# Kernel optimization log

Measured on AMD Instinct MI355X. Metric: run time of the kernel, lower is better.

Reference implementation:

```python
import jax, jax.numpy as jnp
import numpy as np

B, NBLK, D, DY, NDIM, NMC, DH = 4096, 12, 2, 2, 24, 256, 100
SQRT3 = 3.0 ** 0.5
G2 = np.array([[1.0, 0.0], [0.5, SQRT3 / 2.0]], dtype=np.float32)
G = jnp.asarray(np.kron(np.eye(NBLK, dtype=np.float32), G2))  # (24,24) block-diag hexagonal generator
LOG_VOL = (NDIM // 2) * float(np.log(SQRT3 / 2.0))  # log sqrt(det(G G^T))


def _lin(x, w, b=None):
    y = x @ w.T
    return y if b is None else y + b


def _hex_quantize(y):
    # Exact nearest-point quantizer for the product-of-A2 (hexagonal) lattice.
    p = y.reshape(y.shape[:-1] + (NDIM // 2, 2))
    off = jnp.array([0.5, SQRT3 / 2.0], dtype=y.dtype)
    def rnd(q):  # round to rectangular sublattice Z x sqrt(3)Z
        return jnp.stack([jnp.round(q[..., 0]), jnp.round(q[..., 1] / SQRT3) * SQRT3], axis=-1)
    c0 = rnd(p)
    c1 = rnd(p - off) + off
    d0 = jnp.sum((p - c0) ** 2, axis=-1)
    d1 = jnp.sum((p - c1) ** 2, axis=-1)
    return jnp.where((d0 <= d1)[..., None], c0, c1).reshape(y.shape)


def _logits_cumulative(v, Hs, bs, fs):
    # compressai-style per-channel monotone cumulative network. v: (..., C) -> (..., C)
    v = v[..., None]  # (..., C, 1)
    for k in range(len(Hs)):
        v = jnp.einsum('coi,...ci->...co', jax.nn.softplus(Hs[k]), v) + bs[k][:, :, 0]
        if k < len(fs):
            v = v + jnp.tanh(fs[k][:, :, 0]) * jnp.tanh(v)
    return v[..., 0]


def setup_inputs() -> dict:
    key = jax.random.key(0)
    ks = iter(jax.random.split(key, 64))
    def nrm(shape, s=1.0):
        return jax.random.normal(next(ks), shape, jnp.float32) * s
    inp = {}
    inp['x'] = nrm((B, NBLK, D))
    inp['y_mean'] = nrm((NBLK, DY))
    inp['u'] = jax.random.uniform(next(ks), (NMC, NDIM), jnp.float32)
    inp['ga_w0'] = nrm((DH, D), D ** -0.5); inp['ga_b0'] = jnp.zeros((DH,), jnp.float32)
    inp['ga_w1'] = nrm((DH, DH), DH ** -0.5); inp['ga_b1'] = jnp.zeros((DH,), jnp.float32)
    inp['ga_w2'] = nrm((DY, DH), DH ** -0.5); inp['ga_b2'] = jnp.zeros((DY,), jnp.float32)
    inp['gs_w0'] = nrm((DH, DY), DY ** -0.5); inp['gs_b0'] = jnp.zeros((DH,), jnp.float32)
    inp['gs_w1'] = nrm((DH, DH), DH ** -0.5); inp['gs_b1'] = jnp.zeros((DH,), jnp.float32)
    inp['gs_w2'] = nrm((D, DH), DH ** -0.5); inp['gs_b2'] = jnp.zeros((D,), jnp.float32)
    inp['gac_w0'] = nrm((DH, NDIM), NDIM ** -0.5)
    inp['gac_w1'] = nrm((DH, DH), DH ** -0.5)
    inp['gac_w2'] = nrm((NDIM, DH), DH ** -0.5)
    inp['gsc_w0'] = nrm((DH, NDIM), NDIM ** -0.5)
    inp['gsc_w1'] = nrm((DH, DH), DH ** -0.5)
    inp['gsc_w2'] = nrm((NDIM, DH), DH ** -0.5)
    # factorized-prior cumulative params, layer dims 1->3->3->3->3->1
    inp['eb_H0'] = nrm((NDIM, 3, 1), 0.5)
    inp['eb_H1'] = nrm((NDIM, 3, 3), 0.5)
    inp['eb_H2'] = nrm((NDIM, 3, 3), 0.5)
    inp['eb_H3'] = nrm((NDIM, 3, 3), 0.5)
    inp['eb_H4'] = nrm((NDIM, 1, 3), 0.5)
    inp['eb_b0'] = nrm((NDIM, 3, 1), 0.5)
    inp['eb_b1'] = nrm((NDIM, 3, 1), 0.5)
    inp['eb_b2'] = nrm((NDIM, 3, 1), 0.5)
    inp['eb_b3'] = nrm((NDIM, 3, 1), 0.5)
    inp['eb_b4'] = nrm((NDIM, 1, 1), 0.5)
    inp['eb_a0'] = nrm((NDIM, 3, 1), 0.5)
    inp['eb_a1'] = nrm((NDIM, 3, 1), 0.5)
    inp['eb_a2'] = nrm((NDIM, 3, 1), 0.5)
    inp['eb_a3'] = nrm((NDIM, 3, 1), 0.5)
    return inp


def reference(x, y_mean, u, ga_w0, ga_b0, ga_w1, ga_b1, ga_w2, ga_b2,
              gs_w0, gs_b0, gs_w1, gs_b1, gs_w2, gs_b2,
              gac_w0, gac_w1, gac_w2, gsc_w0, gsc_w1, gsc_w2,
              eb_H0, eb_H1, eb_H2, eb_H3, eb_H4,
              eb_b0, eb_b1, eb_b2, eb_b3, eb_b4,
              eb_a0, eb_a1, eb_a2, eb_a3):
    lrelu, sp = jax.nn.leaky_relu, jax.nn.softplus
    # analysis transform g_a: (B, 12, 2) -> (B, 12, dy)
    y1 = _lin(lrelu(_lin(lrelu(_lin(x, ga_w0, ga_b0)), ga_w1, ga_b1)), ga_w2, ga_b2)
    # EMA zero-mean update (buffer assignment => no gradient through the mean)
    ym = jax.lax.stop_gradient(0.05 * y_mean + 0.95 * jnp.mean(y1, axis=0))
    y1 = (y1 - ym).reshape(B, NDIM)
    # coupled analysis transform g_a_c (Softplus MLP, no bias)
    y1 = _lin(sp(_lin(sp(_lin(y1, gac_w0)), gac_w1)), gac_w2)
    # quasi-uniform samples from the Voronoi cell of the lattice origin
    u2 = u @ G
    u2 = u2 - _hex_quantize(u2)
    # lattice quantization with straight-through estimator
    y_q = _hex_quantize(y1)
    y_hat = y1 + jax.lax.stop_gradient(y_q - y1)
    # Monte-Carlo log-likelihood over the Voronoi cell with factorized prior density
    Hs = (eb_H0, eb_H1, eb_H2, eb_H3, eb_H4)
    bs = (eb_b0, eb_b1, eb_b2, eb_b3, eb_b4)
    fs = (eb_a0, eb_a1, eb_a2, eb_a3)
    pts = y_hat[:, None, :] + u2[None, :, :]  # (B, NMC, NDIM)
    def cdf(p):
        return jax.nn.sigmoid(_logits_cumulative(p, Hs, bs, fs))
    _, pdf = jax.jvp(cdf, (pts,), (jnp.ones_like(pts),))  # density = d/dx cdf(x)
    logp = jnp.sum(jnp.log(pdf + 1e-9), axis=-1)  # (B, NMC)
    lik = jax.scipy.special.logsumexp(logp, axis=1) - jnp.log(jnp.float32(NMC)) + LOG_VOL  # (B,)
    # synthesis transforms
    y_hat1 = _lin(sp(_lin(sp(_lin(y_hat, gsc_w0)), gsc_w1)), gsc_w2).reshape(B, NBLK, DY) + ym
    x_hat = _lin(lrelu(_lin(lrelu(_lin(y_hat1, gs_w0, gs_b0)), gs_w1, gs_b1)), gs_w2, gs_b2)
    return (x_hat, lik)
```

## Files before the change

### kernel.cpp

```cpp
#include <hip/hip_runtime.h>
#include <hip/hip_bf16.h>
#include <math.h>
#include <limits.h>

constexpr int NB    = 4096;
constexpr int ROWS2 = NB * 12;
constexpr int G2_BLOCKS = ROWS2 / 64;
constexpr int TBL_CAP = 48;

constexpr size_t WS_Y1    = 0;
constexpr size_t WS_YHAT  = 98304;
constexpr size_t WS_YHAT1 = 196608;
constexpr size_t WS_YM    = 294912;
constexpr size_t WS_U2T   = 294936;
constexpr size_t WS_EB    = 301080;
constexpr size_t WS_KMM   = 302472;
constexpr size_t WS_PART  = 302520;
constexpr size_t WS_W1T   = 320952;
constexpr size_t WS_TBL   = 372152;
constexpr size_t WS_END   = WS_TBL + 24 * TBL_CAP * 256;

constexpr float STEP_ODD = 0.8660254037844386f;
constexpr float INV_ODD  = 1.1547005383792517f;

__device__ __forceinline__ float lrelu(float x) { return x >= 0.f ? x : 0.01f * x; }
__device__ __forceinline__ float rcp_fast(float x) { return __builtin_amdgcn_rcpf(x); }

__device__ __forceinline__ float tanh_fast(float x) {
    float xx = fminf(fmaxf(x, -15.f), 15.f);
    float e = __expf(xx + xx);
    return fmaf(-2.f, rcp_fast(e + 1.f), 1.f);
}
__device__ __forceinline__ float splus(float x) {
    return fmaxf(x, 0.f) + __logf(1.f + __expf(-fabsf(x)));
}
__device__ __forceinline__ float splus_precise(float x) {
    return fmaxf(x, 0.f) + log1pf(expf(-fabsf(x)));
}

__device__ __forceinline__ void fma4(float4& a, float h, const float4& w) {
    a.x = fmaf(h, w.x, a.x); a.y = fmaf(h, w.y, a.y);
    a.z = fmaf(h, w.z, a.z); a.w = fmaf(h, w.w, a.w);
}

__device__ __forceinline__ void hexq(float p0, float p1, float& q0, float& q1) {
    const float S3 = 1.7320508075688772f;
    const float H3 = 0.8660254037844386f;
    float c00 = rintf(p0);
    float c01 = rintf(p1 / S3) * S3;
    float c10 = rintf(p0 - 0.5f) + 0.5f;
    float c11 = rintf((p1 - H3) / S3) * S3 + H3;
    float d0 = (p0 - c00) * (p0 - c00) + (p1 - c01) * (p1 - c01);
    float d1 = (p0 - c10) * (p0 - c10) + (p1 - c11) * (p1 - c11);
    bool take0 = d0 <= d1;
    q0 = take0 ? c00 : c10;
    q1 = take0 ? c01 : c11;
}

__device__ __forceinline__ float logpdf_ch(const float* __restrict__ P, float p) {
    float w00 = P[0], w01 = P[1], w02 = P[2];
    float z0 = fmaf(w00, p, P[3]);
    float z1 = fmaf(w01, p, P[4]);
    float z2 = fmaf(w02, p, P[5]);
    float a0 = P[6], a1 = P[7], a2 = P[8];
    float e0 = tanh_fast(z0), e1 = tanh_fast(z1), e2 = tanh_fast(z2);
    float h0 = fmaf(a0, e0, z0), h1 = fmaf(a1, e1, z1), h2 = fmaf(a2, e2, z2);
    float t0 = w00 * fmaf(a0, fmaf(-e0, e0, 1.f), 1.f);
    float t1 = w01 * fmaf(a1, fmaf(-e1, e1, 1.f), 1.f);
    float t2 = w02 * fmaf(a2, fmaf(-e2, e2, 1.f), 1.f);

#define EB_LAYER(O)                                                            \
    {                                                                          \
        float z0n = fmaf(P[O+0], h0, fmaf(P[O+1], h1, fmaf(P[O+2], h2, P[O+9])));  \
        float z1n = fmaf(P[O+3], h0, fmaf(P[O+4], h1, fmaf(P[O+5], h2, P[O+10]))); \
        float z2n = fmaf(P[O+6], h0, fmaf(P[O+7], h1, fmaf(P[O+8], h2, P[O+11]))); \
        float s0 = fmaf(P[O+0], t0, fmaf(P[O+1], t1, P[O+2] * t2));            \
        float s1 = fmaf(P[O+3], t0, fmaf(P[O+4], t1, P[O+5] * t2));            \
        float s2 = fmaf(P[O+6], t0, fmaf(P[O+7], t1, P[O+8] * t2));            \
        float g0 = P[O+12], g1 = P[O+13], g2 = P[O+14];                        \
        float q0 = tanh_fast(z0n), q1 = tanh_fast(z1n), q2 = tanh_fast(z2n);   \
        h0 = fmaf(g0, q0, z0n); h1 = fmaf(g1, q1, z1n); h2 = fmaf(g2, q2, z2n); \
        t0 = s0 * fmaf(g0, fmaf(-q0, q0, 1.f), 1.f);                           \
        t1 = s1 * fmaf(g1, fmaf(-q1, q1, 1.f), 1.f);                           \
        t2 = s2 * fmaf(g2, fmaf(-q2, q2, 1.f), 1.f);                           \
    }
    EB_LAYER(9)
    EB_LAYER(24)
    EB_LAYER(39)
#undef EB_LAYER

    float L = fmaf(P[54], h0, fmaf(P[55], h1, fmaf(P[56], h2, P[57])));
    float T = fmaf(P[54], t0, fmaf(P[55], t1, P[56] * t2));
    float Lc = fminf(fmaxf(L, -30.f), 30.f);
    float sg = rcp_fast(1.f + __expf(-Lc));
    float pdf = sg * (1.f - sg) * T;
    return __logf(pdf + 1e-9f);
}

__global__ __launch_bounds__(256) void k_prep(
    const float* __restrict__ H0p, const float* __restrict__ H1p,
    const float* __restrict__ H2p, const float* __restrict__ H3p,
    const float* __restrict__ H4p,
    const float* __restrict__ b0p, const float* __restrict__ b1p,
    const float* __restrict__ b2p, const float* __restrict__ b3p,
    const float* __restrict__ b4p,
    const float* __restrict__ a0p, const float* __restrict__ a1p,
    const float* __restrict__ a2p, const float* __restrict__ a3p,
    const float* __restrict__ u,
    const float* __restrict__ w1ga, const float* __restrict__ w1gac,
    const float* __restrict__ w1gsc, const float* __restrict__ w1gs,
    float* __restrict__ eb, float* __restrict__ u2t,
    int* __restrict__ kmm, float* __restrict__ w1t)
{
    int tid = threadIdx.x;
    if (blockIdx.x > 0) {
        int t = blockIdx.x - 1;
        int m = t / 50;
        int o = (t % 50) * 256 + tid;
        int k = o >> 7, i = o & 127;
        const float* src = (m == 0) ? w1ga : (m == 1) ? w1gac
                         : (m == 2) ? w1gsc : w1gs;
        w1t[m * 12800 + o] = (i < 100) ? src[i * 100 + k] : 0.f;
        return;
    }
    if (tid < 24) {
        int c = tid;
        float* P = eb + c * 58;
        for (int j = 0; j < 3; ++j) P[j]      = splus_precise(H0p[c*3+j]);
        for (int j = 0; j < 3; ++j) P[3+j]    = b0p[c*3+j];
        for (int j = 0; j < 3; ++j) P[6+j]    = tanhf(a0p[c*3+j]);
        for (int j = 0; j < 9; ++j) P[9+j]    = splus_precise(H1p[c*9+j]);
        for (int j = 0; j < 3; ++j) P[18+j]   = b1p[c*3+j];
        for (int j = 0; j < 3; ++j) P[21+j]   = tanhf(a1p[c*3+j]);
        for (int j = 0; j < 9; ++j) P[24+j]   = splus_precise(H2p[c*9+j]);
        for (int j = 0; j < 3; ++j) P[33+j]   = b2p[c*3+j];
        for (int j = 0; j < 3; ++j) P[36+j]   = tanhf(a2p[c*3+j]);
        for (int j = 0; j < 9; ++j) P[39+j]   = splus_precise(H3p[c*9+j]);
        for (int j = 0; j < 3; ++j) P[48+j]   = b3p[c*3+j];
        for (int j = 0; j < 3; ++j) P[51+j]   = tanhf(a3p[c*3+j]);
        for (int j = 0; j < 3; ++j) P[54+j]   = splus_precise(H4p[c*3+j]);
        P[57] = b4p[c];
        kmm[tid]      = INT_MAX;
        kmm[24 + tid] = INT_MIN;
    }
    int m = tid;
    if (m < 256) {
        for (int j = 0; j < 12; ++j) {
            float a  = u[m*24 + 2*j];
            float bb = u[m*24 + 2*j + 1];
            float p0 = fmaf(0.5f, bb, a);
            float p1 = 0.8660254037844386f * bb;
            float q0, q1; hexq(p0, p1, q0, q1);
            u2t[(2*j)   * 256 + m] = p0 - q0;
            u2t[(2*j+1) * 256 + m] = p1 - q1;
        }
    }
}

template <int MEAN>
__device__ __forceinline__ void gemm2_body(
    int bid,
    const float* __restrict__ in,
    const float* __restrict__ w0, const float* __restrict__ b0,
    const float* __restrict__ w1t,
    const float* __restrict__ b1, const float* __restrict__ w2,
    const float* __restrict__ b2,
    float* __restrict__ out, float* __restrict__ partial)
{
    __shared__ alignas(16) float shT[100 * 64];
    __shared__ float S[64][2];

    int tid = threadIdx.x;
    int row0 = bid * 64;

    int lrow = tid & 63, jg = tid >> 6;
    float2 xv = ((const float2*)in)[row0 + lrow];
#pragma unroll
    for (int jj = 0; jj < 25; ++jj) {
        int j = jg * 25 + jj;
        shT[j * 64 + lrow] =
            lrelu(fmaf(w0[2*j], xv.x, fmaf(w0[2*j+1], xv.y, b0[j])));
    }

    int lane = tid & 63, wv = tid >> 6;
    int ct = lane & 31;
    int rt = wv * 2 + (lane >> 5);
    bool cvalid = (4 * ct < 100);
    float4 zero4 = make_float4(0.f, 0.f, 0.f, 0.f);
    float4 b14 = cvalid ? *(const float4*)(b1 + 4*ct) : zero4;
    float4 w20 = cvalid ? *(const float4*)(w2 + 4*ct) : zero4;
    float4 w21 = cvalid ? *(const float4*)(w2 + 100 + 4*ct) : zero4;
    __syncthreads();

    float4 acc[8];
#pragma unroll
    for (int r = 0; r < 8; ++r) acc[r] = zero4;
    const float4* wg  = (const float4*)w1t + ct;
    const float4* hT4 = (const float4*)shT;
#pragma unroll 4
    for (int k = 0; k < 100; ++k) {
        float4 w4 = wg[k * 32];
        float4 ha = hT4[k * 16 + rt * 2];
        float4 hb = hT4[k * 16 + rt * 2 + 1];
        fma4(acc[0], ha.x, w4); fma4(acc[1], ha.y, w4);
        fma4(acc[2], ha.z, w4); fma4(acc[3], ha.w, w4);
        fma4(acc[4], hb.x, w4); fma4(acc[5], hb.y, w4);
        fma4(acc[6], hb.z, w4); fma4(acc[7], hb.w, w4);
    }
    __syncthreads();

    float* red = shT;
#pragma unroll
    for (int r = 0; r < 8; ++r) {
        float a0 = lrelu(acc[r].x + b14.x);
        float a1 = lrelu(acc[r].y + b14.y);
        float a2 = lrelu(acc[r].z + b14.z);
        float a3 = lrelu(acc[r].w + b14.w);
        float y0 = fmaf(a0, w20.x, fmaf(a1, w20.y, fmaf(a2, w20.z, a3 * w20.w)));
        float y1 = fmaf(a0, w21.x, fmaf(a1, w21.y, fmaf(a2, w21.z, a3 * w21.w)));
        int row = rt * 8 + r;
        red[(row * 2) * 32 + ct]     = y0;
        red[(row * 2 + 1) * 32 + ct] = y1;
    }
    __syncthreads();
    if (tid < 128) {
        int row = tid >> 1, p = tid & 1;
        const float4* rp = (const float4*)&red[(row * 2 + p) * 32];
        float s = 0.f;
#pragma unroll
        for (int g = 0; g < 8; ++g) {
            float4 v = rp[g];
            s += (v.x + v.y) + (v.z + v.w);
        }
        float y = s + b2[p];
        out[(row0 + row) * 2 + p] = y;
        if (MEAN) S[row][p] = y;
    }
    if (MEAN) {
        __syncthreads();
        if (tid < 24) {
            int j = tid >> 1, par = tid & 1;
            int base = row0 % 12;
            int k0 = (j - base + 12) % 12;
            float s = 0.f;
            for (int k = k0; k < 64; k += 12) s += S[k][par];
            partial[bid * 24 + tid] = s;
        }
    }
}

__global__ __launch_bounds__(256, 4) void k_gemm2_mean(
    const float* __restrict__ in,
    const float* __restrict__ w0, const float* __restrict__ b0,
    const float* __restrict__ w1t,
    const float* __restrict__ b1, const float* __restrict__ w2,
    const float* __restrict__ b2,
    float* __restrict__ out, float* __restrict__ partial)
{
    gemm2_body<1>(blockIdx.x, in, w0, b0, w1t, b1, w2, b2, out, partial);
}

__global__ __launch_bounds__(256) void k_mean_final(
    const float* __restrict__ partial, const float* __restrict__ y_mean,
    float* __restrict__ ym)
{
    int tid = threadIdx.x;
    int c = tid >> 3, s = tid & 7;
    float v = 0.f;
    if (c < 24)
        for (int g = s; g < G2_BLOCKS; g += 8) v += partial[g * 24 + c];
    v += __shfl_xor(v, 1); v += __shfl_xor(v, 2); v += __shfl_xor(v, 4);
    if (c < 24 && s == 0)
        ym[c] = fmaf(0.05f, y_mean[c], 0.95f * (v * (1.0f / NB)));
}

__global__ __launch_bounds__(256, 4) void k_fused24(
    const float* __restrict__ y1,
    const float* __restrict__ w0A, const float* __restrict__ w1tA,
    const float* __restrict__ w2A,
    const float* __restrict__ w0B, const float* __restrict__ w1tB,
    const float* __restrict__ w2B,
    const float* __restrict__ ymg,
    float* __restrict__ yhat, float* __restrict__ yhat1,
    int* __restrict__ kmm)
{
    __shared__ float sw0[2400];
    __shared__ float sw2[2400];
    __shared__ float sX[8 * 25];
    __shared__ float sO[8 * 25];
    __shared__ alignas(16) float h0[100 * 8];
    __shared__ float h1[100 * 8];
    __shared__ float symL[24];
    __shared__ int kminL[24], kmaxL[24];

    int tid = threadIdx.x;
    int row0 = blockIdx.x * 8;

    if (tid < 24) {
        symL[tid] = ymg[tid];
        kminL[tid] = INT_MAX; kmaxL[tid] = INT_MIN;
    }
    __syncthreads();
    for (int e = tid; e < 192; e += 256) {
        int r = e / 24, c = e - r * 24;
        sX[r * 25 + c] = y1[row0 * 24 + e] - symL[c];
    }

    int ii = tid & 127, rg = tid >> 7;

    for (int pass = 0; pass < 2; ++pass) {
        const float* w0  = pass ? w0B  : w0A;
        const float* w1t = pass ? w1tB : w1tA;
        const float* w2  = pass ? w2B  : w2A;
        for (int t = tid; t < 2400; t += 256) {
            sw0[t] = w0[t];
            sw2[t] = w2[t];
        }
        __syncthreads();

        for (int e = tid; e < 800; e += 256) {
            int j = e >> 3, r = e & 7;
            const float* wr = sw0 + j * 24;
            const float* xr = sX + r * 25;
            float a = 0.f, b = 0.f;
#pragma unroll
            for (int k = 0; k < 24; k += 2) {
                a = fmaf(wr[k],     xr[k],     a);
                b = fmaf(wr[k + 1], xr[k + 1], b);
            }
            h0[j * 8 + r] = splus(a + b);
        }
        __syncthreads();

        {
            float4 a = make_float4(0.f, 0.f, 0.f, 0.f);
            const float* wc = w1t + ii;
            const float4* h4 = (const float4*)h0 + rg;
#pragma unroll 4
            for (int j = 0; j < 100; ++j) {
                float w = wc[j * 128];
                float4 h = h4[j * 2];
                a.x = fmaf(w, h.x, a.x); a.y = fmaf(w, h.y, a.y);
                a.z = fmaf(w, h.z, a.z); a.w = fmaf(w, h.w, a.w);
            }
            if (ii < 100) {
                h1[ii * 8 + rg * 4]     = splus(a.x);
                h1[ii * 8 + rg * 4 + 1] = splus(a.y);
                h1[ii * 8 + rg * 4 + 2] = splus(a.z);
                h1[ii * 8 + rg * 4 + 3] = splus(a.w);
            }
        }
        __syncthreads();

        if (tid < 192) {
            int c = tid >> 3, r = tid & 7;
            const float* w2r = sw2 + c * 100;
            float s = 0.f, s2 = 0.f;
#pragma unroll 4
            for (int i = 0; i < 100; i += 2) {
                s  = fmaf(w2r[i],     h1[i * 8 + r],       s);
                s2 = fmaf(w2r[i + 1], h1[(i + 1) * 8 + r], s2);
            }
            float v = s + s2;
            if (pass == 0) sO[r * 25 + c] = v;
            else yhat1[(row0 + r) * 24 + c] = v + symL[c];
        }

        if (pass == 0) {
            __syncthreads();
            if (tid < 96) {
                int pr = tid >> 3, r = tid & 7;
                float v0 = sO[r * 25 + 2*pr], v1 = sO[r * 25 + 2*pr + 1];
                float q0, q1; hexq(v0, v1, q0, q1);
                yhat[(row0 + r) * 24 + 2*pr]     = q0;
                yhat[(row0 + r) * 24 + 2*pr + 1] = q1;
                sX[r * 25 + 2*pr]     = q0;
                sX[r * 25 + 2*pr + 1] = q1;
                int k0 = (int)rintf(q0 * 2.0f);
                int k1 = (int)rintf(q1 * INV_ODD);
                atomicMin(&kminL[2*pr], k0);     atomicMax(&kmaxL[2*pr], k0);
                atomicMin(&kminL[2*pr + 1], k1); atomicMax(&kmaxL[2*pr + 1], k1);
            }
        }
    }
    __syncthreads();
    if (tid < 24) {
        atomicMin(&kmm[tid], kminL[tid]);
        atomicMax(&kmm[24 + tid], kmaxL[tid]);
    }
}

__global__ __launch_bounds__(256, 4) void k_gs_table(
    const float* __restrict__ yhat1,
    const float* __restrict__ w0, const float* __restrict__ b0,
    const float* __restrict__ w1t,
    const float* __restrict__ b1, const float* __restrict__ w2,
    const float* __restrict__ b2, float* __restrict__ xhat,
    const float* __restrict__ eb, const float* __restrict__ u2t,
    const int* __restrict__ kmm, float* __restrict__ tbl)
{
    if (blockIdx.x < (unsigned)G2_BLOCKS) {
        gemm2_body<0>(blockIdx.x, yhat1, w0, b0, w1t, b1, w2, b2, xhat, nullptr);
    } else {
        int cv = blockIdx.x - G2_BLOCKS;
        int c = cv / TBL_CAP, v = cv - c * TBL_CAP;
        int m = threadIdx.x;
        float step = (c & 1) ? STEP_ODD : 0.5f;
        float val = (float)(kmm[c] + v) * step;
        float p = val + u2t[c * 256 + m];
        tbl[cv * 256 + m] = logpdf_ch(eb + c * 58, p);
    }
}

__global__ __launch_bounds__(256) void k_mc_tbl(
    const float* __restrict__ yhat, const float* __restrict__ u2t,
    const float* __restrict__ eb, const int* __restrict__ kmm,
    const float* __restrict__ tbl, float* __restrict__ lik)
{
    __shared__ float redm[4], reds[4];
    int tid = threadIdx.x;
    int wv = tid >> 6;
    int b = blockIdx.x;

    float y[24];
    const float4* yr = (const float4*)(yhat + b * 24);
#pragma unroll
    for (int k4 = 0; k4 < 6; ++k4) {
        float4 t = yr[k4];
        y[4*k4] = t.x; y[4*k4+1] = t.y; y[4*k4+2] = t.z; y[4*k4+3] = t.w;
    }

    float lp = 0.f;
    unsigned miss = 0;
#pragma unroll
    for (int c = 0; c < 24; ++c) {
        float inv = (c & 1) ? INV_ODD : 2.0f;
        int k = (int)rintf(y[c] * inv);
        int idx = k - kmm[c];
        if (idx >= 0 && idx < TBL_CAP)
            lp += tbl[(c * TBL_CAP + idx) * 256 + tid];
        else
            miss |= (1u << c);
    }
    while (miss) {
        int c = __ffs(miss) - 1;
        miss &= miss - 1;
        lp += logpdf_ch(eb + c * 58, y[c] + u2t[c * 256 + tid]);
    }

    float m = lp;
#pragma unroll
    for (int off = 1; off < 64; off <<= 1) m = fmaxf(m, __shfl_xor(m, off));
    if ((tid & 63) == 0) redm[wv] = m;
    __syncthreads();
    float mx = fmaxf(fmaxf(redm[0], redm[1]), fmaxf(redm[2], redm[3]));
    float e = __expf(lp - mx);
#pragma unroll
    for (int off = 1; off < 64; off <<= 1) e += __shfl_xor(e, off);
    if ((tid & 63) == 0) reds[wv] = e;
    __syncthreads();
    if (tid == 0)
        lik[b] = mx + __logf(reds[0] + reds[1] + reds[2] + reds[3])
               - 7.271269879190247f;
}

__global__ __launch_bounds__(256) void k_mc_direct(
    const float* __restrict__ yhat, const float* __restrict__ u2t,
    const float* __restrict__ eb, float* __restrict__ lik)
{
    __shared__ alignas(16) float sU[24 * 256];
    __shared__ float redm[4], reds[4];
    int tid = threadIdx.x;
    int wv = tid >> 6;
    int b = blockIdx.x;
    for (int i = tid; i < 1536; i += 256)
        ((float4*)sU)[i] = ((const float4*)u2t)[i];
    __syncthreads();

    float lp = 0.f;
    for (int c = 0; c < 24; ++c)
        lp += logpdf_ch(eb + c * 58, yhat[b * 24 + c] + sU[c * 256 + tid]);

    float m = lp;
#pragma unroll
    for (int off = 1; off < 64; off <<= 1) m = fmaxf(m, __shfl_xor(m, off));
    if ((tid & 63) == 0) redm[wv] = m;
    __syncthreads();
    float mx = fmaxf(fmaxf(redm[0], redm[1]), fmaxf(redm[2], redm[3]));
    float e = __expf(lp - mx);
#pragma unroll
    for (int off = 1; off < 64; off <<= 1) e += __shfl_xor(e, off);
    if ((tid & 63) == 0) reds[wv] = e;
    __syncthreads();
    if (tid == 0)
        lik[b] = mx + __logf(reds[0] + reds[1] + reds[2] + reds[3])
               - 7.271269879190247f;
}

extern "C" void kernel_launch(void* const* d_in, const int* in_sizes, int n_in,
                              void* d_out, int out_size, void* d_ws, size_t ws_size,
                              hipStream_t stream)
{
    (void)in_sizes; (void)n_in; (void)out_size;
    const float* x      = (const float*)d_in[0];
    const float* y_mean = (const float*)d_in[1];
    const float* u      = (const float*)d_in[2];
    const float* ga_w0  = (const float*)d_in[3];
    const float* ga_b0  = (const float*)d_in[4];
    const float* ga_w1  = (const float*)d_in[5];
    const float* ga_b1  = (const float*)d_in[6];
    const float* ga_w2  = (const float*)d_in[7];
    const float* ga_b2  = (const float*)d_in[8];
    const float* gs_w0  = (const float*)d_in[9];
    const float* gs_b0  = (const float*)d_in[10];
    const float* gs_w1  = (const float*)d_in[11];
    const float* gs_b1  = (const float*)d_in[12];
    const float* gs_w2  = (const float*)d_in[13];
    const float* gs_b2  = (const float*)d_in[14];
    const float* gac_w0 = (const float*)d_in[15];
    const float* gac_w1 = (const float*)d_in[16];
    const float* gac_w2 = (const float*)d_in[17];
    const float* gsc_w0 = (const float*)d_in[18];
    const float* gsc_w1 = (const float*)d_in[19];
    const float* gsc_w2 = (const float*)d_in[20];
    const float* eb_H0  = (const float*)d_in[21];
    const float* eb_H1  = (const float*)d_in[22];
    const float* eb_H2  = (const float*)d_in[23];
    const float* eb_H3  = (const float*)d_in[24];
    const float* eb_H4  = (const float*)d_in[25];
    const float* eb_b0  = (const float*)d_in[26];
    const float* eb_b1  = (const float*)d_in[27];
    const float* eb_b2  = (const float*)d_in[28];
    const float* eb_b3  = (const float*)d_in[29];
    const float* eb_b4  = (const float*)d_in[30];
    const float* eb_a0  = (const float*)d_in[31];
    const float* eb_a1  = (const float*)d_in[32];
    const float* eb_a2  = (const float*)d_in[33];
    const float* eb_a3  = (const float*)d_in[34];

    float* ws    = (float*)d_ws;
    float* y1    = ws + WS_Y1;
    float* yhat  = ws + WS_YHAT;
    float* yhat1 = ws + WS_YHAT1;
    float* ym    = ws + WS_YM;
    float* u2t   = ws + WS_U2T;
    float* eb    = ws + WS_EB;
    int*   kmm   = (int*)(ws + WS_KMM);
    float* part  = ws + WS_PART;
    float* w1t   = ws + WS_W1T;
    float* tbl   = ws + WS_TBL;
    float* xhat  = (float*)d_out;
    float* lik   = (float*)d_out + 98304;

    float* w1tGA  = w1t;
    float* w1tGAC = w1t + 12800;
    float* w1tGSC = w1t + 25600;
    float* w1tGS  = w1t + 38400;

    bool use_tbl = ws_size >= WS_END * sizeof(float);

    k_prep<<<201, 256, 0, stream>>>(eb_H0, eb_H1, eb_H2, eb_H3, eb_H4,
                                    eb_b0, eb_b1, eb_b2, eb_b3, eb_b4,
                                    eb_a0, eb_a1, eb_a2, eb_a3, u,
                                    ga_w1, gac_w1, gsc_w1, gs_w1,
                                    eb, u2t, kmm, w1t);
    k_gemm2_mean<<<G2_BLOCKS, 256, 0, stream>>>(x, ga_w0, ga_b0, w1tGA,
                                                ga_b1, ga_w2, ga_b2, y1, part);
    k_mean_final<<<1, 256, 0, stream>>>(part, y_mean, ym);
    k_fused24<<<NB / 8, 256, 0, stream>>>(y1, gac_w0, w1tGAC, gac_w2,
                                          gsc_w0, w1tGSC, gsc_w2,
                                          ym, yhat, yhat1, kmm);
    if (use_tbl) {
        k_gs_table<<<G2_BLOCKS + 24 * TBL_CAP, 256, 0, stream>>>(
            yhat1, gs_w0, gs_b0, w1tGS, gs_b1, gs_w2, gs_b2, xhat,
            eb, u2t, kmm, tbl);
        k_mc_tbl<<<NB, 256, 0, stream>>>(yhat, u2t, eb, kmm, tbl, lik);
    } else {
        k_gs_table<<<G2_BLOCKS, 256, 0, stream>>>(
            yhat1, gs_w0, gs_b0, w1tGS, gs_b1, gs_w2, gs_b2, xhat,
            eb, u2t, kmm, tbl);
        k_mc_direct<<<NB, 256, 0, stream>>>(yhat, u2t, eb, lik);
    }
}
```

Before: 140.2 us.

## Use fixed-range logpdf table and build it alongside the analysis GEMM

The logpdf lookup table now covers a fixed lattice index range starting at KBASE=-32 with 64 entries, instead of a data-dependent min/max range gathered with atomics. Because the range no longer depends on the quantized latents, the table can be built in the first GEMM kernel's extra blocks rather than after k_fused24. This removes the shared and global atomics and the kmm bookkeeping, and lets table construction overlap earlier work. The cost is a larger table (64 vs 48 entries per channel). Values outside the fixed range still fall back to direct evaluation, so correctness holds, but fallbacks become more frequent if latents exceed that range.

```diff
diff --git a/kernel.cpp b/kernel.cpp
--- a/kernel.cpp
+++ b/kernel.cpp
@@ -6,7 +6,8 @@
 constexpr int NB    = 4096;
 constexpr int ROWS2 = NB * 12;
 constexpr int G2_BLOCKS = ROWS2 / 64;
-constexpr int TBL_CAP = 48;
+constexpr int TBL_CAP = 64;
+constexpr int KBASE   = -32;
 
 constexpr size_t WS_Y1    = 0;
 constexpr size_t WS_YHAT  = 98304;
@@ -14,10 +15,9 @@
 constexpr size_t WS_YM    = 294912;
 constexpr size_t WS_U2T   = 294936;
 constexpr size_t WS_EB    = 301080;
-constexpr size_t WS_KMM   = 302472;
-constexpr size_t WS_PART  = 302520;
-constexpr size_t WS_W1T   = 320952;
-constexpr size_t WS_TBL   = 372152;
+constexpr size_t WS_PART  = 302472;
+constexpr size_t WS_W1T   = 320904;
+constexpr size_t WS_TBL   = 372104;
 constexpr size_t WS_END   = WS_TBL + 24 * TBL_CAP * 256;
 
 constexpr float STEP_ODD = 0.8660254037844386f;
@@ -110,7 +110,7 @@
     const float* __restrict__ w1ga, const float* __restrict__ w1gac,
     const float* __restrict__ w1gsc, const float* __restrict__ w1gs,
     float* __restrict__ eb, float* __restrict__ u2t,
-    int* __restrict__ kmm, float* __restrict__ w1t)
+    float* __restrict__ w1t)
 {
     int tid = threadIdx.x;
     if (blockIdx.x > 0) {
@@ -140,8 +140,6 @@
         for (int j = 0; j < 3; ++j) P[51+j]   = tanhf(a3p[c*3+j]);
         for (int j = 0; j < 3; ++j) P[54+j]   = splus_precise(H4p[c*3+j]);
         P[57] = b4p[c];
-        kmm[tid]      = INT_MAX;
-        kmm[24 + tid] = INT_MIN;
     }
     int m = tid;
     if (m < 256) {
@@ -249,15 +247,27 @@
     }
 }
 
-__global__ __launch_bounds__(256, 4) void k_gemm2_mean(
+__global__ __launch_bounds__(256, 4) void k_ga_table(
     const float* __restrict__ in,
     const float* __restrict__ w0, const float* __restrict__ b0,
     const float* __restrict__ w1t,
     const float* __restrict__ b1, const float* __restrict__ w2,
     const float* __restrict__ b2,
-    float* __restrict__ out, float* __restrict__ partial)
-{
-    gemm2_body<1>(blockIdx.x, in, w0, b0, w1t, b1, w2, b2, out, partial);
+    float* __restrict__ out, float* __restrict__ partial,
+    const float* __restrict__ eb, const float* __restrict__ u2t,
+    float* __restrict__ tbl)
+{
+    if (blockIdx.x < (unsigned)G2_BLOCKS) {
+        gemm2_body<1>(blockIdx.x, in, w0, b0, w1t, b1, w2, b2, out, partial);
+    } else {
+        int cv = blockIdx.x - G2_BLOCKS;
+        int c = cv >> 6, v = cv & 63;
+        int m = threadIdx.x;
+        float step = (c & 1) ? STEP_ODD : 0.5f;
+        float val = (float)(KBASE + v) * step;
+        float p = val + u2t[c * 256 + m];
+        tbl[cv * 256 + m] = logpdf_ch(eb + c * 58, p);
+    }
 }
 
 __global__ __launch_bounds__(256) void k_mean_final(
@@ -281,8 +291,7 @@
     const float* __restrict__ w0B, const float* __restrict__ w1tB,
     const float* __restrict__ w2B,
     const float* __restrict__ ymg,
-    float* __restrict__ yhat, float* __restrict__ yhat1,
-    int* __restrict__ kmm)
+    float* __restrict__ yhat, float* __restrict__ yhat1)
 {
     __shared__ float sw0[2400];
     __shared__ float sw2[2400];
@@ -291,15 +300,11 @@
     __shared__ alignas(16) float h0[100 * 8];
     __shared__ float h1[100 * 8];
     __shared__ float symL[24];
-    __shared__ int kminL[24], kmaxL[24];
 
     int tid = threadIdx.x;
     int row0 = blockIdx.x * 8;
 
-    if (tid < 24) {
-        symL[tid] = ymg[tid];
-        kminL[tid] = INT_MAX; kmaxL[tid] = INT_MIN;
-    }
+    if (tid < 24) symL[tid] = ymg[tid];
     __syncthreads();
     for (int e = tid; e < 192; e += 256) {
         int r = e / 24, c = e - r * 24;
@@ -376,45 +381,24 @@
                 yhat[(row0 + r) * 24 + 2*pr + 1] = q1;
                 sX[r * 25 + 2*pr]     = q0;
                 sX[r * 25 + 2*pr + 1] = q1;
-                int k0 = (int)rintf(q0 * 2.0f);
-                int k1 = (int)rintf(q1 * INV_ODD);
-                atomicMin(&kminL[2*pr], k0);     atomicMax(&kmaxL[2*pr], k0);
-                atomicMin(&kminL[2*pr + 1], k1); atomicMax(&kmaxL[2*pr + 1], k1);
             }
         }
     }
-    __syncthreads();
-    if (tid < 24) {
-        atomicMin(&kmm[tid], kminL[tid]);
-        atomicMax(&kmm[24 + tid], kmaxL[tid]);
-    }
-}
-
-__global__ __launch_bounds__(256, 4) void k_gs_table(
+}
+
+__global__ __launch_bounds__(256, 4) void k_gs(
     const float* __restrict__ yhat1,
     const float* __restrict__ w0, const float* __restrict__ b0,
     const float* __restrict__ w1t,
     const float* __restrict__ b1, const float* __restrict__ w2,
-    const float* __restrict__ b2, float* __restrict__ xhat,
-    const float* __restrict__ eb, const float* __restrict__ u2t,
-    const int* __restrict__ kmm, float* __restrict__ tbl)
-{
-    if (blockIdx.x < (unsigned)G2_BLOCKS) {
-        gemm2_body<0>(blockIdx.x, yhat1, w0, b0, w1t, b1, w2, b2, xhat, nullptr);
-    } else {
-        int cv = blockIdx.x - G2_BLOCKS;
-        int c = cv / TBL_CAP, v = cv - c * TBL_CAP;
-        int m = threadIdx.x;
-        float step = (c & 1) ? STEP_ODD : 0.5f;
-        float val = (float)(kmm[c] + v) * step;
-        float p = val + u2t[c * 256 + m];
-        tbl[cv * 256 + m] = logpdf_ch(eb + c * 58, p);
-    }
+    const float* __restrict__ b2, float* __restrict__ xhat)
+{
+    gemm2_body<0>(blockIdx.x, yhat1, w0, b0, w1t, b1, w2, b2, xhat, nullptr);
 }
 
 __global__ __launch_bounds__(256) void k_mc_tbl(
     const float* __restrict__ yhat, const float* __restrict__ u2t,
-    const float* __restrict__ eb, const int* __restrict__ kmm,
+    const float* __restrict__ eb,
     const float* __restrict__ tbl, float* __restrict__ lik)
 {
     __shared__ float redm[4], reds[4];
@@ -436,7 +420,7 @@
     for (int c = 0; c < 24; ++c) {
         float inv = (c & 1) ? INV_ODD : 2.0f;
         int k = (int)rintf(y[c] * inv);
-        int idx = k - kmm[c];
+        int idx = k - KBASE;
         if (idx >= 0 && idx < TBL_CAP)
             lp += tbl[(c * TBL_CAP + idx) * 256 + tid];
         else
@@ -545,7 +529,6 @@
     float* ym    = ws + WS_YM;
     float* u2t   = ws + WS_U2T;
     float* eb    = ws + WS_EB;
-    int*   kmm   = (int*)(ws + WS_KMM);
     float* part  = ws + WS_PART;
     float* w1t   = ws + WS_W1T;
     float* tbl   = ws + WS_TBL;
@@ -563,22 +546,23 @@
                                     eb_b0, eb_b1, eb_b2, eb_b3, eb_b4,
                                     eb_a0, eb_a1, eb_a2, eb_a3, u,
                                     ga_w1, gac_w1, gsc_w1, gs_w1,
-                                    eb, u2t, kmm, w1t);
-    k_gemm2_mean<<<G2_BLOCKS, 256, 0, stream>>>(x, ga_w0, ga_b0, w1tGA,
-                                                ga_b1, ga_w2, ga_b2, y1, part);
+                                    eb, u2t, w1t);
+    if (use_tbl)
+        k_ga_table<<<G2_BLOCKS + 24 * TBL_CAP, 256, 0, stream>>>(
+            x, ga_w0, ga_b0, w1tGA, ga_b1, ga_w2, ga_b2, y1, part,
+            eb, u2t, tbl);
+    else
+        k_ga_table<<<G2_BLOCKS, 256, 0, stream>>>(
+            x, ga_w0, ga_b0, w1tGA, ga_b1, ga_w2, ga_b2, y1, part,
+            eb, u2t, tbl);
     k_mean_final<<<1, 256, 0, stream>>>(part, y_mean, ym);
     k_fused24<<<NB / 8, 256, 0, stream>>>(y1, gac_w0, w1tGAC, gac_w2,
                                           gsc_w0, w1tGSC, gsc_w2,
-                                          ym, yhat, yhat1, kmm);
-    if (use_tbl) {
-        k_gs_table<<<G2_BLOCKS + 24 * TBL_CAP, 256, 0, stream>>>(
-            yhat1, gs_w0, gs_b0, w1tGS, gs_b1, gs_w2, gs_b2, xhat,
-            eb, u2t, kmm, tbl);
-        k_mc_tbl<<<NB, 256, 0, stream>>>(yhat, u2t, eb, kmm, tbl, lik);
-    } else {
-        k_gs_table<<<G2_BLOCKS, 256, 0, stream>>>(
-            yhat1, gs_w0, gs_b0, w1tGS, gs_b1, gs_w2, gs_b2, xhat,
-            eb, u2t, kmm, tbl);
+                                          ym, yhat, yhat1);
+    k_gs<<<G2_BLOCKS, 256, 0, stream>>>(yhat1, gs_w0, gs_b0, w1tGS,
+                                        gs_b1, gs_w2, gs_b2, xhat);
+    if (use_tbl)
+        k_mc_tbl<<<NB, 256, 0, stream>>>(yhat, u2t, eb, tbl, lik);
+    else
         k_mc_direct<<<NB, 256, 0, stream>>>(yhat, u2t, eb, lik);
-    }
-}
+}
```

Measured after the change: 131.9 us. 1.06x faster.
